# Kernel optimization log

Measured on AMD Instinct MI355X. Metric: run time of the kernel, lower is better.

## Reference

```python
import jax, jax.numpy as jnp
import numpy as np

N = 100_000      # nodes
E = 1_600_000    # edges (avg degree 16)
F_IN = 128       # in_feats
H = 128          # n_hidden
H2 = 64          # n_hidden // 2


def setup_inputs() -> dict:
    key = jax.random.key(0)
    k1, k2, k3, k4, k5 = jax.random.split(key, 5)
    features = jax.random.normal(k1, (N, F_IN), dtype=jnp.float32)
    W1 = jax.random.normal(k2, (F_IN, H), dtype=jnp.float32) * 0.05
    W2 = jax.random.normal(k3, (H, H2), dtype=jnp.float32) * 0.05
    src = jax.random.randint(k4, (E,), 0, N, dtype=jnp.int32)
    dst = jax.random.randint(k5, (E,), 0, N, dtype=jnp.int32)
    return {"features": features, "W1": W1, "W2": W2, "src": src, "dst": dst}


def _graph_conv(h, W, src, dst, out_norm, in_norm):
    # DGL GraphConv, norm='both', bias=False:
    #   rst = D_dst^{-1/2} * (A @ (D_src^{-1/2} * h)) @ W
    # (weight applied before/after aggregation is mathematically identical)
    h = h * out_norm[:, None]                                   # scale source feats
    agg = jax.ops.segment_sum(h[src], dst, num_segments=N)      # SpMM: sum over in-edges
    return (agg * in_norm[:, None]) @ W


def reference(features, W1, W2, src, dst):
    ones = jnp.ones(src.shape[0], dtype=jnp.float32)
    # allow_zero_in_degree=True -> DGL clamps degrees to min 1 for norm
    out_deg = jnp.clip(jax.ops.segment_sum(ones, src, num_segments=N), 1.0)
    in_deg = jnp.clip(jax.ops.segment_sum(ones, dst, num_segments=N), 1.0)
    out_norm = out_deg ** -0.5
    in_norm = in_deg ** -0.5
    h = _graph_conv(features, W1, src, dst, out_norm, in_norm)  # [N, H]
    h = jax.nn.relu(h)
    return _graph_conv(h, W2, src, dst, out_norm, in_norm)      # [N, H2]
```

## Files before the change

### kernel.cpp

```cpp
#include <hip/hip_runtime.h>
#include <cstdint>
#include <cstddef>

#define NN 100000
#define NE 1600000
#define FD 128
#define HD2 64

#define BSH 7
#define BSZ 128
#define NB ((NN + BSZ - 1) / BSZ)
#define TILE 4096
#define NTILE ((NE + TILE - 1) / TILE)
#define CAPB 2560
#define NPREP ((NN * 32 + FD * 64 + HD2 * 64 + 255) / 256)

static_assert(NB <= 1024, "bucket scan assumes <=1024 buckets");

typedef short bf16x8_t __attribute__((ext_vector_type(8)));
typedef float f32x4_t __attribute__((ext_vector_type(4)));

static __device__ __forceinline__ uint f2bf(float x) {
  uint u = __float_as_uint(x);
  return (u + 0x7fffu + ((u >> 16) & 1u)) >> 16;
}
static __device__ __forceinline__ uint pack2(float lo, float hi) {
  return f2bf(lo) | (f2bf(hi) << 16);
}
static __device__ __forceinline__ float bflo(uint v) { return __uint_as_float(v << 16); }
static __device__ __forceinline__ float bfhi(uint v) { return __uint_as_float(v & 0xffff0000u); }

static __device__ __forceinline__ float dec_w(uint r) {
  return __uint_as_float(((r >> 17) + 0x38000u) << 12);
}

__global__ void k_bucket_prep(const int* __restrict__ src, const int* __restrict__ dst,
                              int* __restrict__ bcnt_d, int* __restrict__ bcnt_s,
                              uint* __restrict__ brec_d, ushort* __restrict__ brec_s,
                              const float* __restrict__ feat, uint* __restrict__ Xraw,
                              const float* __restrict__ W1, const float* __restrict__ W2,
                              uint* __restrict__ W1t, uint* __restrict__ W2t) {
  __shared__ int h[NB], gb[NB];
  const int bid = blockIdx.x;
  if (bid >= 2 * NTILE) {
    int i = (bid - 2 * NTILE) * 256 + threadIdx.x;
    if (i < NN * 32) {
      float4 f = *(const float4*)(feat + 4 * (size_t)i);
      uint2 o;
      o.x = pack2(f.x, f.y);
      o.y = pack2(f.z, f.w);
      *(uint2*)(Xraw + 2 * (size_t)i) = o;
    } else {
      int j = i - NN * 32;
      if (j < FD * 64) {
        int n = j >> 6, kk = j & 63;
        W1t[j] = pack2(W1[(size_t)(2 * kk) * FD + n], W1[(size_t)(2 * kk + 1) * FD + n]);
      } else if (j < FD * 64 + HD2 * 64) {
        int j2 = j - FD * 64;
        int n = j2 >> 6, kk = j2 & 63;
        W2t[j2] = pack2(W2[(size_t)(2 * kk) * HD2 + n], W2[(size_t)(2 * kk + 1) * HD2 + n]);
      }
    }
    return;
  }
  const bool is_dst = bid < NTILE;
  const int* key = is_dst ? dst : src;
  const int base = (is_dst ? bid : bid - NTILE) * TILE;
  for (int i = threadIdx.x; i < NB; i += 256) h[i] = 0;
  __syncthreads();
  for (int i = threadIdx.x; i < TILE; i += 256) {
    int e = base + i;
    if (e < NE) atomicAdd(&h[key[e] >> BSH], 1);
  }
  __syncthreads();
  int* bcnt = is_dst ? bcnt_d : bcnt_s;
  for (int i = threadIdx.x; i < NB; i += 256) {
    int c = h[i];
    gb[i] = c ? atomicAdd(bcnt + i, c) : 0;
    h[i] = 0;
  }
  __syncthreads();
  if (is_dst) {
    for (int i = threadIdx.x; i < TILE; i += 256) {
      int e = base + i;
      if (e < NE) {
        int d = dst[e], sv = src[e];
        int bd = d >> BSH;
        int rd = gb[bd] + atomicAdd(&h[bd], 1);
        if (rd < CAPB)
          brec_d[(size_t)bd * CAPB + rd] = ((uint)(d & (BSZ - 1)) << 17) | (uint)sv;
      }
    }
  } else {
    for (int i = threadIdx.x; i < TILE; i += 256) {
      int e = base + i;
      if (e < NE) {
        int sv = src[e];
        int bs = sv >> BSH;
        int rs = gb[bs] + atomicAdd(&h[bs], 1);
        if (rs < CAPB)
          brec_s[(size_t)bs * CAPB + rs] = (ushort)(sv & (BSZ - 1));
      }
    }
  }
}

__global__ __launch_bounds__(1024) void k_onorm_scan(const ushort* __restrict__ brec_s,
                                                     const int* __restrict__ bcnt_s,
                                                     float* __restrict__ out_norm,
                                                     const int* __restrict__ bcnt_d,
                                                     int* __restrict__ boff_d) {
  __shared__ int sm[1024];
  const int t = threadIdx.x;
  const int b = blockIdx.x;
  if (b < NB) {
    if (t < BSZ) sm[t] = 0;
    __syncthreads();
    const int len = min(bcnt_s[b], CAPB);
    const size_t rbase = (size_t)b * CAPB;
    for (int e = t; e < len; e += 1024)
      atomicAdd(&sm[brec_s[rbase + e]], 1);
    __syncthreads();
    const int s0 = b * BSZ;
    const int ns = min(BSZ, NN - s0);
    if (t < ns) out_norm[s0 + t] = rsqrtf((float)max(sm[t], 1));
  } else {
    int v = (t < NB) ? bcnt_d[t] : 0;
    sm[t] = v;
    __syncthreads();
#pragma unroll
    for (int off = 1; off < 1024; off <<= 1) {
      int x = (t >= off) ? sm[t - off] : 0;
      __syncthreads();
      sm[t] += x;
      __syncthreads();
    }
    if (t < NB) boff_d[t + 1] = sm[t];
    if (t == 0) boff_d[0] = 0;
  }
}

__global__ __launch_bounds__(256) void k_build(const uint* __restrict__ brec_d,
                                               const int* __restrict__ bcnt_d,
                                               const int* __restrict__ boff,
                                               const float* __restrict__ onorm,
                                               int* __restrict__ row_ptr,
                                               float* __restrict__ in_norm,
                                               uint* __restrict__ csr) {
  __shared__ int lcnt[BSZ];
  __shared__ int lscan[BSZ + 1];
  __shared__ int lcur[BSZ];
  __shared__ int lcsr[CAPB];
  const int t = threadIdx.x;
  const int b = blockIdx.x;
  const int d0 = b * BSZ;
  const int nd = min(BSZ, NN - d0);
  const size_t rbase = (size_t)b * CAPB;
  const int len = min(bcnt_d[b], CAPB);
  const int ebase = boff[b];

  for (int i = t; i < BSZ; i += 256) lcnt[i] = 0;
  __syncthreads();
  for (int e = t; e < len; e += 256)
    atomicAdd(&lcnt[brec_d[rbase + e] >> 17], 1);
  __syncthreads();
  for (int i = t; i < nd; i += 256)
    in_norm[d0 + i] = rsqrtf((float)max(lcnt[i], 1));

  if (t < BSZ) lcur[t] = lcnt[t];
  __syncthreads();
#pragma unroll
  for (int off = 1; off < BSZ; off <<= 1) {
    int x = (t >= off && t < BSZ) ? lcur[t - off] : 0;
    __syncthreads();
    if (t < BSZ) lcur[t] += x;
    __syncthreads();
  }
  if (t < BSZ) lscan[t + 1] = lcur[t];
  if (t == 0) lscan[0] = 0;
  __syncthreads();
  for (int i = t; i <= nd; i += 256) row_ptr[d0 + i] = ebase + lscan[i];
  if (t < BSZ) lcur[t] = lscan[t];
  __syncthreads();

  for (int e = t; e < len; e += 256) {
    uint r = brec_d[rbase + e];
    int p = atomicAdd(&lcur[r >> 17], 1);
    lcsr[p] = (int)(r & 0x1FFFFu);
  }
  __syncthreads();
  for (int ld = t; ld < nd; ld += 256) {
    int a = lscan[ld], bnd = lscan[ld + 1];
    for (int i = a + 1; i < bnd; ++i) {
      int v = lcsr[i];
      int j = i - 1;
      while (j >= a && lcsr[j] > v) { lcsr[j + 1] = lcsr[j]; --j; }
      lcsr[j + 1] = v;
    }
  }
  __syncthreads();
  for (int i = t; i < len; i += 256) {
    int s = lcsr[i];
    uint code = (__float_as_uint(onorm[s]) >> 12) - 0x38000u;
    csr[ebase + i] = (code << 17) | (uint)s;
  }
}

__global__ void k_spmm1b(const uint* __restrict__ Xraw, const int* __restrict__ row_ptr,
                         const uint* __restrict__ csr, const float* __restrict__ in_norm,
                         uint* __restrict__ Hb1) {
  int gid = blockIdx.x * blockDim.x + threadIdx.x;
  int row = gid >> 6;
  if (row >= NN) return;
  int lane = threadIdx.x & 63;
  int grp = lane >> 4;
  int gl = lane & 15;
  int e0 = row_ptr[row], e1 = row_ptr[row + 1];
  float2 a0 = {0.f, 0.f}, a1 = {0.f, 0.f}, a2 = {0.f, 0.f}, a3 = {0.f, 0.f};
#define ACCW(v, ww)                                                       \
  a0.x = fmaf(ww, bflo((v).x), a0.x); a0.y = fmaf(ww, bfhi((v).x), a0.y); \
  a1.x = fmaf(ww, bflo((v).y), a1.x); a1.y = fmaf(ww, bfhi((v).y), a1.y); \
  a2.x = fmaf(ww, bflo((v).z), a2.x); a2.y = fmaf(ww, bfhi((v).z), a2.y); \
  a3.x = fmaf(ww, bflo((v).w), a3.x); a3.y = fmaf(ww, bfhi((v).w), a3.y);
  int e = e0;
  for (; e + 16 <= e1; e += 16) {
    uint r0 = csr[e + grp];
    uint r1 = csr[e + 4 + grp];
    uint r2 = csr[e + 8 + grp];
    uint r3 = csr[e + 12 + grp];
    uint4 v0 = *(const uint4*)(Xraw + ((size_t)(r0 & 0x1FFFFu) << 6) + (gl << 2));
    uint4 v1 = *(const uint4*)(Xraw + ((size_t)(r1 & 0x1FFFFu) << 6) + (gl << 2));
    uint4 v2 = *(const uint4*)(Xraw + ((size_t)(r2 & 0x1FFFFu) << 6) + (gl << 2));
    uint4 v3 = *(const uint4*)(Xraw + ((size_t)(r3 & 0x1FFFFu) << 6) + (gl << 2));
    float w0 = dec_w(r0), w1 = dec_w(r1), w2 = dec_w(r2), w3 = dec_w(r3);
    ACCW(v0, w0);
    ACCW(v1, w1);
    ACCW(v2, w2);
    ACCW(v3, w3);
  }
  for (; e + 4 <= e1; e += 4) {
    uint r0 = csr[e + grp];
    uint4 v0 = *(const uint4*)(Xraw + ((size_t)(r0 & 0x1FFFFu) << 6) + (gl << 2));
    float w0 = dec_w(r0);
    ACCW(v0, w0);
  }
  if (e + grp < e1) {
    uint r0 = csr[e + grp];
    uint4 v0 = *(const uint4*)(Xraw + ((size_t)(r0 & 0x1FFFFu) << 6) + (gl << 2));
    float w0 = dec_w(r0);
    ACCW(v0, w0);
  }
#undef ACCW
#pragma unroll
  for (int m = 16; m <= 32; m <<= 1) {
    a0.x += __shfl_xor(a0.x, m); a0.y += __shfl_xor(a0.y, m);
    a1.x += __shfl_xor(a1.x, m); a1.y += __shfl_xor(a1.y, m);
    a2.x += __shfl_xor(a2.x, m); a2.y += __shfl_xor(a2.y, m);
    a3.x += __shfl_xor(a3.x, m); a3.y += __shfl_xor(a3.y, m);
  }
  if (grp == 0) {
    float wi = in_norm[row];
    uint4 o;
    o.x = pack2(a0.x * wi, a0.y * wi);
    o.y = pack2(a1.x * wi, a1.y * wi);
    o.z = pack2(a2.x * wi, a2.y * wi);
    o.w = pack2(a3.x * wi, a3.y * wi);
    *(uint4*)(Hb1 + ((size_t)row << 6) + (gl << 2)) = o;
  }
}

__global__ __launch_bounds__(256) void k_mlp(const uint* __restrict__ Hb1,
                                             const uint* __restrict__ W1t,
                                             const uint* __restrict__ W2t,
                                             const float* __restrict__ onorm,
                                             ushort* __restrict__ Tb) {
  __shared__ ushort h_lds[64 * FD];
  char* const lds = (char*)h_lds;
  const int tid = threadIdx.x;
  const int wid = tid >> 6;
  const int lane = tid & 63;
  const int l15 = lane & 15;
  const int g = lane >> 4;
  const int rowbase = blockIdx.x * 64 + wid * 16;

  const int ar = min(rowbase + l15, NN - 1);
  const uint* Arow = Hb1 + (size_t)ar * 64;
  bf16x8_t afr[4];
#pragma unroll
  for (int kc = 0; kc < 4; ++kc)
    afr[kc] = *(const bf16x8_t*)(Arow + kc * 16 + g * 4);

  float wnorm[4];
#pragma unroll
  for (int r = 0; r < 4; ++r)
    wnorm[r] = onorm[min(rowbase + 4 * g + r, NN - 1)];

#pragma unroll
  for (int nf = 0; nf < 8; ++nf) {
    f32x4_t acc = {0.f, 0.f, 0.f, 0.f};
#pragma unroll
    for (int kc = 0; kc < 4; ++kc) {
      bf16x8_t b = *(const bf16x8_t*)(W1t + (size_t)(nf * 16 + l15) * 64 + kc * 16 + g * 4);
      acc = __builtin_amdgcn_mfma_f32_16x16x32_bf16(afr[kc], b, acc, 0, 0, 0);
    }
#pragma unroll
    for (int r = 0; r < 4; ++r) {
      float hv = fmaxf(acc[r], 0.f) * wnorm[r];
      int row = wid * 16 + 4 * g + r;
      int byte = row * 256 + (nf * 16 + l15) * 2;
      byte ^= (row & 7) << 4;
      *(ushort*)(lds + byte) = (ushort)f2bf(hv);
    }
  }
  __syncthreads();

  bf16x8_t a2[4];
#pragma unroll
  for (int kc = 0; kc < 4; ++kc) {
    int row = wid * 16 + l15;
    int byte = row * 256 + (kc * 32 + 8 * g) * 2;
    byte ^= (row & 7) << 4;
    a2[kc] = *(const bf16x8_t*)(lds + byte);
  }
#pragma unroll
  for (int nf = 0; nf < 4; ++nf) {
    f32x4_t acc = {0.f, 0.f, 0.f, 0.f};
#pragma unroll
    for (int kc = 0; kc < 4; ++kc) {
      bf16x8_t b = *(const bf16x8_t*)(W2t + (size_t)(nf * 16 + l15) * 64 + kc * 16 + g * 4);
      acc = __builtin_amdgcn_mfma_f32_16x16x32_bf16(a2[kc], b, acc, 0, 0, 0);
    }
#pragma unroll
    for (int r = 0; r < 4; ++r) {
      int row = rowbase + 4 * g + r;
      if (row < NN)
        Tb[(size_t)row * HD2 + nf * 16 + l15] = (ushort)f2bf(acc[r]);
    }
  }
}

__global__ void k_spmm2b(const uint* __restrict__ Tb, const int* __restrict__ row_ptr,
                         const uint* __restrict__ csr, const float* __restrict__ in_norm,
                         float* __restrict__ out) {
  int gid = blockIdx.x * blockDim.x + threadIdx.x;
  int row = gid >> 6;
  if (row >= NN) return;
  int lane = threadIdx.x & 63;
  int grp = lane >> 4;
  int gl = lane & 15;
  int e0 = row_ptr[row], e1 = row_ptr[row + 1];
  float2 a0 = {0.f, 0.f}, a1 = {0.f, 0.f};
#define ACC2(v)                                  \
  a0.x += bflo((v).x); a0.y += bfhi((v).x);      \
  a1.x += bflo((v).y); a1.y += bfhi((v).y);
  int e = e0;
  for (; e + 16 <= e1; e += 16) {
    uint s0 = csr[e + grp] & 0x1FFFFu;
    uint s1 = csr[e + 4 + grp] & 0x1FFFFu;
    uint s2 = csr[e + 8 + grp] & 0x1FFFFu;
    uint s3 = csr[e + 12 + grp] & 0x1FFFFu;
    uint2 v0 = *(const uint2*)(Tb + ((size_t)s0 << 5) + (gl << 1));
    uint2 v1 = *(const uint2*)(Tb + ((size_t)s1 << 5) + (gl << 1));
    uint2 v2 = *(const uint2*)(Tb + ((size_t)s2 << 5) + (gl << 1));
    uint2 v3 = *(const uint2*)(Tb + ((size_t)s3 << 5) + (gl << 1));
    ACC2(v0);
    ACC2(v1);
    ACC2(v2);
    ACC2(v3);
  }
  for (; e + 4 <= e1; e += 4) {
    uint s0 = csr[e + grp] & 0x1FFFFu;
    uint2 v0 = *(const uint2*)(Tb + ((size_t)s0 << 5) + (gl << 1));
    ACC2(v0);
  }
  if (e + grp < e1) {
    uint s0 = csr[e + grp] & 0x1FFFFu;
    uint2 v0 = *(const uint2*)(Tb + ((size_t)s0 << 5) + (gl << 1));
    ACC2(v0);
  }
#undef ACC2
#pragma unroll
  for (int m = 16; m <= 32; m <<= 1) {
    a0.x += __shfl_xor(a0.x, m); a0.y += __shfl_xor(a0.y, m);
    a1.x += __shfl_xor(a1.x, m); a1.y += __shfl_xor(a1.y, m);
  }
  if (grp == 0) {
    float wi = in_norm[row];
    *(float4*)(out + (size_t)row * HD2 + gl * 4) =
        make_float4(a0.x * wi, a0.y * wi, a1.x * wi, a1.y * wi);
  }
}

extern "C" void kernel_launch(void* const* d_in, const int* in_sizes, int n_in,
                              void* d_out, int out_size, void* d_ws, size_t ws_size,
                              hipStream_t stream) {
  const float* feat = (const float*)d_in[0];
  const float* W1   = (const float*)d_in[1];
  const float* W2   = (const float*)d_in[2];
  const int*   src  = (const int*)d_in[3];
  const int*   dst  = (const int*)d_in[4];
  float* out = (float*)d_out;

  char* p = (char*)d_ws;
  auto take = [&p](size_t bytes) -> char* {
    char* r = p;
    p += (bytes + 511) & ~(size_t)511;
    return r;
  };
  int*   row_ptr  = (int*)take((size_t)(NN + 1) * 4);
  int*   bcnt     = (int*)take((size_t)2 * NB * 4);
  int*   boff_d   = (int*)take((size_t)(NB + 1) * 4);
  float* out_norm = (float*)take((size_t)NN * 4);
  float* in_norm  = (float*)take((size_t)NN * 4);
  uint*  csr      = (uint*)take((size_t)NE * 4);
  uint*  W1t      = (uint*)take((size_t)FD * 64 * 4);
  uint*  W2t      = (uint*)take((size_t)HD2 * 64 * 4);
  uint*  Xraw     = (uint*)take((size_t)NN * 64 * 4);
  uint*  Hb1      = (uint*)take((size_t)NN * 64 * 4);
  int*   bcnt_d   = bcnt;
  int*   bcnt_s   = bcnt + NB;
  ushort* Tb      = (ushort*)Xraw;
  uint*   brec_d  = (uint*)Hb1;
  ushort* brec_s  = (ushort*)(Hb1 + (size_t)NB * CAPB);

  hipMemsetAsync(bcnt, 0, (size_t)2 * NB * 4, stream);

  k_bucket_prep<<<2 * NTILE + NPREP, 256, 0, stream>>>(src, dst, bcnt_d, bcnt_s, brec_d, brec_s,
                                                       feat, Xraw, W1, W2, W1t, W2t);
  k_onorm_scan <<<NB + 1, 1024, 0, stream>>>(brec_s, bcnt_s, out_norm, bcnt_d, boff_d);
  k_build      <<<NB, 256, 0, stream>>>(brec_d, bcnt_d, boff_d, out_norm,
                                        row_ptr, in_norm, csr);

  k_spmm1b<<<(NN * 64) / 256, 256, 0, stream>>>(Xraw, row_ptr, csr, in_norm, Hb1);
  k_mlp   <<<(NN + 63) / 64, 256, 0, stream>>>(Hb1, W1t, W2t, out_norm, Tb);
  k_spmm2b<<<(NN * 64) / 256, 256, 0, stream>>>((const uint*)Tb, row_ptr, csr, in_norm, out);
}
```

Measured before the change: 270.3 us.

## Stage bucket records in LDS and write them out contiguously per bucket

The bucketing kernel now runs a block-local prefix scan over bucket counts and first places each edge record into a shared-memory array sorted by bucket. It then writes the records to global memory in bucket order, so consecutive threads store to consecutive addresses instead of scattering one store per edge. The source-bucket records also shrink from 16-bit to 8-bit. In exchange the kernel uses about 24 KB of LDS per block (up from about 6 KB), which can lower occupancy, and adds a 256-step scan with several extra barriers.

After: 256.2 us (median of 2 runs). 5.2% less time.

```diff
diff --git a/kernel.cpp b/kernel.cpp
--- a/kernel.cpp
+++ b/kernel.cpp
@@ -19,6 +19,7 @@
 
 typedef short bf16x8_t __attribute__((ext_vector_type(8)));
 typedef float f32x4_t __attribute__((ext_vector_type(4)));
+typedef unsigned char uchar;
 
 static __device__ __forceinline__ uint f2bf(float x) {
   uint u = __float_as_uint(x);
@@ -36,14 +37,21 @@
 
 __global__ void k_bucket_prep(const int* __restrict__ src, const int* __restrict__ dst,
                               int* __restrict__ bcnt_d, int* __restrict__ bcnt_s,
-                              uint* __restrict__ brec_d, ushort* __restrict__ brec_s,
+                              uint* __restrict__ brec_d, uchar* __restrict__ brec_s,
                               const float* __restrict__ feat, uint* __restrict__ Xraw,
                               const float* __restrict__ W1, const float* __restrict__ W2,
                               uint* __restrict__ W1t, uint* __restrict__ W2t) {
-  __shared__ int h[NB], gb[NB];
+  __shared__ int h[NB];
+  __shared__ int gb[NB];
+  __shared__ int ls[NB];
+  __shared__ int psum[256];
+  __shared__ int ntot;
+  __shared__ ushort bkt[TILE];
+  __shared__ uint lrec[TILE];
   const int bid = blockIdx.x;
+  const int t = threadIdx.x;
   if (bid >= 2 * NTILE) {
-    int i = (bid - 2 * NTILE) * 256 + threadIdx.x;
+    int i = (bid - 2 * NTILE) * 256 + t;
     if (i < NN * 32) {
       float4 f = *(const float4*)(feat + 4 * (size_t)i);
       uint2 o;
@@ -66,46 +74,83 @@
   const bool is_dst = bid < NTILE;
   const int* key = is_dst ? dst : src;
   const int base = (is_dst ? bid : bid - NTILE) * TILE;
-  for (int i = threadIdx.x; i < NB; i += 256) h[i] = 0;
-  __syncthreads();
-  for (int i = threadIdx.x; i < TILE; i += 256) {
+  for (int i = t; i < NB; i += 256) h[i] = 0;
+  __syncthreads();
+  for (int i = t; i < TILE; i += 256) {
     int e = base + i;
     if (e < NE) atomicAdd(&h[key[e] >> BSH], 1);
   }
   __syncthreads();
   int* bcnt = is_dst ? bcnt_d : bcnt_s;
-  for (int i = threadIdx.x; i < NB; i += 256) {
+  for (int i = t; i < NB; i += 256) {
     int c = h[i];
     gb[i] = c ? atomicAdd(bcnt + i, c) : 0;
-    h[i] = 0;
-  }
+  }
+  int i0 = t * 4;
+  int c0 = (i0 + 0 < NB) ? h[i0 + 0] : 0;
+  int c1 = (i0 + 1 < NB) ? h[i0 + 1] : 0;
+  int c2 = (i0 + 2 < NB) ? h[i0 + 2] : 0;
+  int c3 = (i0 + 3 < NB) ? h[i0 + 3] : 0;
+  int cs = c0 + c1 + c2 + c3;
+  psum[t] = cs;
+  __syncthreads();
+#pragma unroll
+  for (int off = 1; off < 256; off <<= 1) {
+    int x = (t >= off) ? psum[t - off] : 0;
+    __syncthreads();
+    psum[t] += x;
+    __syncthreads();
+  }
+  int excl = psum[t] - cs;
+  if (i0 + 0 < NB) ls[i0 + 0] = excl;
+  if (i0 + 1 < NB) ls[i0 + 1] = excl + c0;
+  if (i0 + 2 < NB) ls[i0 + 2] = excl + c0 + c1;
+  if (i0 + 3 < NB) ls[i0 + 3] = excl + c0 + c1 + c2;
+  if (t == 255) ntot = psum[255];
+  __syncthreads();
+  for (int i = t; i < NB; i += 256) h[i] = 0;
   __syncthreads();
   if (is_dst) {
-    for (int i = threadIdx.x; i < TILE; i += 256) {
+    for (int i = t; i < TILE; i += 256) {
       int e = base + i;
       if (e < NE) {
         int d = dst[e], sv = src[e];
-        int bd = d >> BSH;
-        int rd = gb[bd] + atomicAdd(&h[bd], 1);
-        if (rd < CAPB)
-          brec_d[(size_t)bd * CAPB + rd] = ((uint)(d & (BSZ - 1)) << 17) | (uint)sv;
+        int b = d >> BSH;
+        int q = ls[b] + atomicAdd(&h[b], 1);
+        lrec[q] = ((uint)(d & (BSZ - 1)) << 17) | (uint)sv;
+        bkt[q] = (ushort)b;
       }
     }
   } else {
-    for (int i = threadIdx.x; i < TILE; i += 256) {
+    for (int i = t; i < TILE; i += 256) {
       int e = base + i;
       if (e < NE) {
         int sv = src[e];
-        int bs = sv >> BSH;
-        int rs = gb[bs] + atomicAdd(&h[bs], 1);
-        if (rs < CAPB)
-          brec_s[(size_t)bs * CAPB + rs] = (ushort)(sv & (BSZ - 1));
+        int b = sv >> BSH;
+        int q = ls[b] + atomicAdd(&h[b], 1);
+        lrec[q] = (uint)(sv & (BSZ - 1));
+        bkt[q] = (ushort)b;
       }
     }
   }
-}
-
-__global__ __launch_bounds__(1024) void k_onorm_scan(const ushort* __restrict__ brec_s,
+  __syncthreads();
+  const int n = ntot;
+  if (is_dst) {
+    for (int q = t; q < n; q += 256) {
+      int b = bkt[q];
+      int p = gb[b] + (q - ls[b]);
+      if (p < CAPB) brec_d[(size_t)b * CAPB + p] = lrec[q];
+    }
+  } else {
+    for (int q = t; q < n; q += 256) {
+      int b = bkt[q];
+      int p = gb[b] + (q - ls[b]);
+      if (p < CAPB) brec_s[(size_t)b * CAPB + p] = (uchar)lrec[q];
+    }
+  }
+}
+
+__global__ __launch_bounds__(1024) void k_onorm_scan(const uchar* __restrict__ brec_s,
                                                      const int* __restrict__ bcnt_s,
                                                      float* __restrict__ out_norm,
                                                      const int* __restrict__ bcnt_d,
@@ -421,7 +466,7 @@
   int*   bcnt_s   = bcnt + NB;
   ushort* Tb      = (ushort*)Xraw;
   uint*   brec_d  = (uint*)Hb1;
-  ushort* brec_s  = (ushort*)(Hb1 + (size_t)NB * CAPB);
+  uchar*  brec_s  = (uchar*)(Hb1 + (size_t)NB * CAPB);
 
   hipMemsetAsync(bcnt, 0, (size_t)2 * NB * 4, stream);
 
```
